# Kernel tuning notes

Measured on AMD Instinct MI355X. Metric: run time of the kernel, lower is better.

The kernel has to match this reference:

```python
import jax, jax.numpy as jnp
import numpy as np

B, N_DIM, K_DIM = 16384, 4096, 128


def setup_inputs() -> dict:
    key = jax.random.key(0)
    k1, k2, k3, k4 = jax.random.split(key, 4)
    x = jax.random.normal(k1, (B, N_DIM), dtype=jnp.float32)
    # nn.Linear(n_dim, 1): weight (1, n_dim), bias (1,)
    lim = 1.0 / np.sqrt(N_DIM)
    W = jax.random.uniform(k2, (1, N_DIM), dtype=jnp.float32, minval=-lim, maxval=lim)
    b = jax.random.uniform(k3, (1,), dtype=jnp.float32, minval=-lim, maxval=lim)
    # V initialized N(0, 0.001)
    V = 0.001 * jax.random.normal(k4, (N_DIM, K_DIM), dtype=jnp.float32)
    return {"x": x, "W": W, "b": b, "V": V}


def reference(x, W, b, V):
    # linear part: (B,1)
    linear = x @ W.T + b
    # term1 = 0.5 * sum_k (x @ V)_k^2  (torch code's 'sum_of_square')
    xv = x @ V  # (B, k)
    term1 = 0.5 * jnp.sum(xv * xv, axis=1, keepdims=True)
    # term2: torch's expand+matmul+bmm reduces algebraically to
    # -0.5 * (sum_i x_i)^2 * ||V.sum(0)||^2  (identical math, no (B,n,n) tensor)
    s = jnp.sum(V, axis=0)  # (k,)
    xsum = jnp.sum(x, axis=1, keepdims=True)  # (B,1)
    term2 = -0.5 * (xsum * xsum) * jnp.dot(s, s)
    return linear + term1 + term2
```

## Files before the change

### kernel.cpp

```cpp
#include <hip/hip_runtime.h>

typedef __bf16 bf16;
typedef __bf16 bf16x8 __attribute__((ext_vector_type(8)));
typedef float f32x16 __attribute__((ext_vector_type(16)));

#define B_ROWS 16384
#define N_DIM  4096
#define K_DIM  128

__global__ __launch_bounds__(256) void prep_kernel(const float* __restrict__ V,
                                                   float* __restrict__ spart,
                                                   bf16* __restrict__ Ut) {
    __shared__ bf16 tile[128 * 136];
    __shared__ float sp[256];
    const int t = threadIdx.x;
    const int jbase = blockIdx.x * 128;
    const int c  = t & 127;
    const int j0 = t >> 7;

    float sacc = 0.f;
#pragma unroll 8
    for (int i = 0; i < 64; ++i) {
        int j = j0 + 2 * i;
        float v = V[(size_t)(jbase + j) * K_DIM + c];
        sacc += v;
        tile[c * 136 + j] = (bf16)v;
    }
    sp[t] = sacc;
    __syncthreads();
    if (t < 128) spart[blockIdx.x * 128 + t] = sp[t] + sp[t + 128];

    const int col = t >> 1, half = t & 1;
#pragma unroll
    for (int i = 0; i < 4; ++i) {
        uint4 d = *(const uint4*)&tile[col * 136 + half * 64 + i * 16];
        *(uint4*)&Ut[(size_t)col * N_DIM + jbase + half * 64 + i * 16] = d;
    }
}

__global__ __launch_bounds__(128) void finalize_s(const float* __restrict__ spart,
                                                  float* __restrict__ snorm_out) {
    const int t = threadIdx.x;
    float s = 0.f;
#pragma unroll
    for (int b = 0; b < 32; ++b) s += spart[b * 128 + t];
    float sq = s * s;
#pragma unroll
    for (int m = 32; m >= 1; m >>= 1) sq += __shfl_down(sq, m, 64);
    __shared__ float red[2];
    if ((t & 63) == 0) red[t >> 6] = sq;
    __syncthreads();
    if (t == 0) snorm_out[0] = red[0] + red[1];
}

__global__ __launch_bounds__(256, 2) void fm_main(const float* __restrict__ x,
                                                  const float* __restrict__ W,
                                                  const float* __restrict__ bptr,
                                                  const bf16* __restrict__ Ut,
                                                  const float* __restrict__ snorm_ptr,
                                                  float* __restrict__ out) {
    __shared__ bf16  xs[32 * 72];
    __shared__ bf16  us[128 * 72];
    __shared__ float redxs[32 * 8];
    __shared__ float redxw[32 * 8];
    __shared__ float rowsq[4 * 32];

    const int t    = threadIdx.x;
    const int wave = t >> 6;
    const int lane = t & 63;
    const int l31  = lane & 31;
    const int h    = lane >> 5;
    const int r0   = blockIdx.x * 32;

    const int srow = t >> 3;
    const int scg  = t & 7;
    const int ucol = t >> 1;
    const int uhalf = t & 1;

    f32x16 acc;
#pragma unroll
    for (int i = 0; i < 16; ++i) acc[i] = 0.f;

    float xsum_acc = 0.f, xw_acc = 0.f;
    const float* xrow = x + (size_t)(r0 + srow) * N_DIM + scg * 8;
    const bf16*  urow = Ut + (size_t)ucol * N_DIM + uhalf * 32;

    for (int kb = 0; kb < N_DIM; kb += 64) {
        float4 a0 = *(const float4*)(xrow + kb);
        float4 a1 = *(const float4*)(xrow + kb + 4);
        float4 w0 = *(const float4*)(W + kb + scg * 8);
        float4 w1 = *(const float4*)(W + kb + scg * 8 + 4);
        const uint4* up = (const uint4*)(urow + kb);
        uint4 u0 = up[0], u1 = up[1], u2 = up[2], u3 = up[3];

        xsum_acc += (a0.x + a0.y + a0.z + a0.w) + (a1.x + a1.y + a1.z + a1.w);
        xw_acc   += a0.x * w0.x + a0.y * w0.y + a0.z * w0.z + a0.w * w0.w
                  + a1.x * w1.x + a1.y * w1.y + a1.z * w1.z + a1.w * w1.w;

        bf16x8 xb;
        xb[0] = (bf16)a0.x; xb[1] = (bf16)a0.y; xb[2] = (bf16)a0.z; xb[3] = (bf16)a0.w;
        xb[4] = (bf16)a1.x; xb[5] = (bf16)a1.y; xb[6] = (bf16)a1.z; xb[7] = (bf16)a1.w;

        __syncthreads();
        *(bf16x8*)&xs[srow * 72 + scg * 8] = xb;
        uint4* usp = (uint4*)&us[ucol * 72 + uhalf * 32];
        usp[0] = u0; usp[1] = u1; usp[2] = u2; usp[3] = u3;
        __syncthreads();

#pragma unroll
        for (int ks = 0; ks < 64; ks += 16) {
            bf16x8 af  = *(const bf16x8*)&xs[l31 * 72 + ks + h * 8];
            bf16x8 bfv = *(const bf16x8*)&us[(wave * 32 + l31) * 72 + ks + h * 8];
            acc = __builtin_amdgcn_mfma_f32_32x32x16_bf16(af, bfv, acc, 0, 0, 0);
        }
    }

    redxs[srow * 8 + scg] = xsum_acc;
    redxw[srow * 8 + scg] = xw_acc;

#pragma unroll
    for (int r = 0; r < 16; ++r) {
        float s = acc[r] * acc[r];
        s += __shfl_xor(s, 1);
        s += __shfl_xor(s, 2);
        s += __shfl_xor(s, 4);
        s += __shfl_xor(s, 8);
        s += __shfl_xor(s, 16);
        if (l31 == 0) {
            int row = (r & 3) + 8 * (r >> 2) + 4 * h;
            rowsq[wave * 32 + row] = s;
        }
    }
    __syncthreads();

    if (t < 32) {
        float xsum = 0.f, xw = 0.f;
#pragma unroll
        for (int g = 0; g < 8; ++g) { xsum += redxs[t * 8 + g]; xw += redxw[t * 8 + g]; }
        float sq = rowsq[t] + rowsq[32 + t] + rowsq[64 + t] + rowsq[96 + t];
        float snorm = snorm_ptr[0];
        float bv = bptr[0];
        out[r0 + t] = bv + xw + 0.5f * sq - 0.5f * xsum * xsum * snorm;
    }
}

extern "C" void kernel_launch(void* const* d_in, const int* in_sizes, int n_in,
                              void* d_out, int out_size, void* d_ws, size_t ws_size,
                              hipStream_t stream) {
    const float* x  = (const float*)d_in[0];
    const float* W  = (const float*)d_in[1];
    const float* bp = (const float*)d_in[2];
    const float* V  = (const float*)d_in[3];
    float* out = (float*)d_out;

    char* ws = (char*)d_ws;
    float* snorm = (float*)ws;
    float* spart = (float*)(ws + 1024);
    bf16*  Ut    = (bf16*)(ws + 32768);

    hipLaunchKernelGGL(prep_kernel, dim3(32), dim3(256), 0, stream, V, spart, Ut);
    hipLaunchKernelGGL(finalize_s, dim3(1), dim3(128), 0, stream, spart, snorm);
    hipLaunchKernelGGL(fm_main, dim3(512), dim3(256), 0, stream, x, W, bp, Ut, snorm, out);
}
```

Measured before the change: 399.8 us.

## Double-buffer LDS tiles and prefetch next x/U tile with direct-to-LDS loads

Converts the main GEMM loop to a double-buffered pipeline. The next x and W slices are prefetched into registers, and the next U tile is loaded straight into LDS with global_load_lds while MFMAs run on the current buffer. This cuts the two barriers per iteration to one and hides global memory latency behind compute. In exchange, the U tile in LDS loses its row padding, so MFMA operand reads may hit bank conflicts. Correctness also relies on the async LDS loads having completed before the barrier.

```diff
diff --git a/kernel.cpp b/kernel.cpp
--- a/kernel.cpp
+++ b/kernel.cpp
@@ -59,10 +59,10 @@
                                                   const bf16* __restrict__ Ut,
                                                   const float* __restrict__ snorm_ptr,
                                                   float* __restrict__ out) {
-    __shared__ bf16  xs[32 * 72];
-    __shared__ bf16  us[128 * 72];
-    __shared__ float redxs[32 * 8];
-    __shared__ float redxw[32 * 8];
+    __shared__ bf16  xs[2][32 * 72];
+    __shared__ bf16  us[2][128 * 64];
+    __shared__ float redxs[256];
+    __shared__ float redxw[256];
     __shared__ float rowsq[4 * 32];
 
     const int t    = threadIdx.x;
@@ -74,8 +74,6 @@
 
     const int srow = t >> 3;
     const int scg  = t & 7;
-    const int ucol = t >> 1;
-    const int uhalf = t & 1;
 
     f32x16 acc;
 #pragma unroll
@@ -83,40 +81,60 @@
 
     float xsum_acc = 0.f, xw_acc = 0.f;
     const float* xrow = x + (size_t)(r0 + srow) * N_DIM + scg * 8;
-    const bf16*  urow = Ut + (size_t)ucol * N_DIM + uhalf * 32;
+    const float* wrow = W + scg * 8;
+    const bf16* ub = Ut + (size_t)(wave * 32 + (lane >> 3)) * N_DIM + (lane & 7) * 8;
 
-    for (int kb = 0; kb < N_DIM; kb += 64) {
-        float4 a0 = *(const float4*)(xrow + kb);
-        float4 a1 = *(const float4*)(xrow + kb + 4);
-        float4 w0 = *(const float4*)(W + kb + scg * 8);
-        float4 w1 = *(const float4*)(W + kb + scg * 8 + 4);
-        const uint4* up = (const uint4*)(urow + kb);
-        uint4 u0 = up[0], u1 = up[1], u2 = up[2], u3 = up[3];
+    float4 a0 = *(const float4*)(xrow);
+    float4 a1 = *(const float4*)(xrow + 4);
+    float4 w0 = *(const float4*)(wrow);
+    float4 w1 = *(const float4*)(wrow + 4);
+#pragma unroll
+    for (int j = 0; j < 4; ++j) {
+        __builtin_amdgcn_global_load_lds(
+            (const __attribute__((address_space(1))) void*)(ub + (size_t)j * 8 * N_DIM),
+            (__attribute__((address_space(3))) void*)&us[0][(wave * 32 + j * 8) * 64],
+            16, 0, 0);
+    }
+
+    for (int it = 0; it < 64; ++it) {
+        const int b = it & 1;
+        const int kb_next = (it < 63) ? (it + 1) * 64 : 0;
+
+        bf16x8 xb;
+        xb[0] = (bf16)a0.x; xb[1] = (bf16)a0.y; xb[2] = (bf16)a0.z; xb[3] = (bf16)a0.w;
+        xb[4] = (bf16)a1.x; xb[5] = (bf16)a1.y; xb[6] = (bf16)a1.z; xb[7] = (bf16)a1.w;
+        *(bf16x8*)&xs[b][srow * 72 + scg * 8] = xb;
+
+        __syncthreads();
+
+        float4 na0 = *(const float4*)(xrow + kb_next);
+        float4 na1 = *(const float4*)(xrow + kb_next + 4);
+        float4 nw0 = *(const float4*)(wrow + kb_next);
+        float4 nw1 = *(const float4*)(wrow + kb_next + 4);
+#pragma unroll
+        for (int j = 0; j < 4; ++j) {
+            __builtin_amdgcn_global_load_lds(
+                (const __attribute__((address_space(1))) void*)(ub + (size_t)j * 8 * N_DIM + kb_next),
+                (__attribute__((address_space(3))) void*)&us[b ^ 1][(wave * 32 + j * 8) * 64],
+                16, 0, 0);
+        }
 
         xsum_acc += (a0.x + a0.y + a0.z + a0.w) + (a1.x + a1.y + a1.z + a1.w);
         xw_acc   += a0.x * w0.x + a0.y * w0.y + a0.z * w0.z + a0.w * w0.w
                   + a1.x * w1.x + a1.y * w1.y + a1.z * w1.z + a1.w * w1.w;
 
-        bf16x8 xb;
-        xb[0] = (bf16)a0.x; xb[1] = (bf16)a0.y; xb[2] = (bf16)a0.z; xb[3] = (bf16)a0.w;
-        xb[4] = (bf16)a1.x; xb[5] = (bf16)a1.y; xb[6] = (bf16)a1.z; xb[7] = (bf16)a1.w;
-
-        __syncthreads();
-        *(bf16x8*)&xs[srow * 72 + scg * 8] = xb;
-        uint4* usp = (uint4*)&us[ucol * 72 + uhalf * 32];
-        usp[0] = u0; usp[1] = u1; usp[2] = u2; usp[3] = u3;
-        __syncthreads();
-
 #pragma unroll
         for (int ks = 0; ks < 64; ks += 16) {
-            bf16x8 af  = *(const bf16x8*)&xs[l31 * 72 + ks + h * 8];
-            bf16x8 bfv = *(const bf16x8*)&us[(wave * 32 + l31) * 72 + ks + h * 8];
+            bf16x8 af  = *(const bf16x8*)&xs[b][l31 * 72 + ks + h * 8];
+            bf16x8 bfv = *(const bf16x8*)&us[b][(wave * 32 + l31) * 64 + ks + h * 8];
             acc = __builtin_amdgcn_mfma_f32_32x32x16_bf16(af, bfv, acc, 0, 0, 0);
         }
+
+        a0 = na0; a1 = na1; w0 = nw0; w1 = nw1;
     }
 
-    redxs[srow * 8 + scg] = xsum_acc;
-    redxw[srow * 8 + scg] = xw_acc;
+    redxs[t] = xsum_acc;
+    redxw[t] = xw_acc;
 
 #pragma unroll
     for (int r = 0; r < 16; ++r) {
```

After: 392.4 us. About the same (-1.9%).

## Load MFMA operands directly from global memory, dropping LDS staging and barriers

Applied to the files above, without the earlier changes.

The main kernel no longer stages x and U tiles through shared memory with two barriers per k-step. Each lane now loads its MFMA fragments directly from global memory into registers, and wave 0 alone computes the row sum and linear dot product. This removes LDS traffic and barriers from the loop. In exchange, every one of the four waves reads the same 32 rows of x, quadrupling x load requests that the cache must absorb, and the per-lane access pattern is strided across rows with less coalescing.

```diff
diff --git a/kernel.cpp b/kernel.cpp
--- a/kernel.cpp
+++ b/kernel.cpp
@@ -59,11 +59,9 @@
                                                   const bf16* __restrict__ Ut,
                                                   const float* __restrict__ snorm_ptr,
                                                   float* __restrict__ out) {
-    __shared__ bf16  xs[32 * 72];
-    __shared__ bf16  us[128 * 72];
-    __shared__ float redxs[32 * 8];
-    __shared__ float redxw[32 * 8];
     __shared__ float rowsq[4 * 32];
+    __shared__ float redx[32];
+    __shared__ float redw[32];
 
     const int t    = threadIdx.x;
     const int wave = t >> 6;
@@ -72,51 +70,48 @@
     const int h    = lane >> 5;
     const int r0   = blockIdx.x * 32;
 
-    const int srow = t >> 3;
-    const int scg  = t & 7;
-    const int ucol = t >> 1;
-    const int uhalf = t & 1;
-
     f32x16 acc;
 #pragma unroll
     for (int i = 0; i < 16; ++i) acc[i] = 0.f;
 
-    float xsum_acc = 0.f, xw_acc = 0.f;
-    const float* xrow = x + (size_t)(r0 + srow) * N_DIM + scg * 8;
-    const bf16*  urow = Ut + (size_t)ucol * N_DIM + uhalf * 32;
+    float xs_acc = 0.f, xw_acc = 0.f;
+
+    const float* xp = x + (size_t)(r0 + l31) * N_DIM + h * 8;
+    const bf16*  up = Ut + (size_t)(wave * 32 + l31) * N_DIM + h * 8;
+    const float* wp = W + h * 8;
 
     for (int kb = 0; kb < N_DIM; kb += 64) {
-        float4 a0 = *(const float4*)(xrow + kb);
-        float4 a1 = *(const float4*)(xrow + kb + 4);
-        float4 w0 = *(const float4*)(W + kb + scg * 8);
-        float4 w1 = *(const float4*)(W + kb + scg * 8 + 4);
-        const uint4* up = (const uint4*)(urow + kb);
-        uint4 u0 = up[0], u1 = up[1], u2 = up[2], u3 = up[3];
+        float4 xa0[4], xa1[4];
+        bf16x8 bfr[4];
+#pragma unroll
+        for (int j = 0; j < 4; ++j) {
+            xa0[j] = *(const float4*)(xp + kb + j * 16);
+            xa1[j] = *(const float4*)(xp + kb + j * 16 + 4);
+            bfr[j] = *(const bf16x8*)(up + kb + j * 16);
+        }
 
-        xsum_acc += (a0.x + a0.y + a0.z + a0.w) + (a1.x + a1.y + a1.z + a1.w);
-        xw_acc   += a0.x * w0.x + a0.y * w0.y + a0.z * w0.z + a0.w * w0.w
-                  + a1.x * w1.x + a1.y * w1.y + a1.z * w1.z + a1.w * w1.w;
-
-        bf16x8 xb;
-        xb[0] = (bf16)a0.x; xb[1] = (bf16)a0.y; xb[2] = (bf16)a0.z; xb[3] = (bf16)a0.w;
-        xb[4] = (bf16)a1.x; xb[5] = (bf16)a1.y; xb[6] = (bf16)a1.z; xb[7] = (bf16)a1.w;
-
-        __syncthreads();
-        *(bf16x8*)&xs[srow * 72 + scg * 8] = xb;
-        uint4* usp = (uint4*)&us[ucol * 72 + uhalf * 32];
-        usp[0] = u0; usp[1] = u1; usp[2] = u2; usp[3] = u3;
-        __syncthreads();
+        if (wave == 0) {
+#pragma unroll
+            for (int j = 0; j < 4; ++j) {
+                float4 w0 = *(const float4*)(wp + kb + j * 16);
+                float4 w1 = *(const float4*)(wp + kb + j * 16 + 4);
+                xs_acc += (xa0[j].x + xa0[j].y + xa0[j].z + xa0[j].w)
+                        + (xa1[j].x + xa1[j].y + xa1[j].z + xa1[j].w);
+                xw_acc += xa0[j].x * w0.x + xa0[j].y * w0.y + xa0[j].z * w0.z + xa0[j].w * w0.w
+                        + xa1[j].x * w1.x + xa1[j].y * w1.y + xa1[j].z * w1.z + xa1[j].w * w1.w;
+            }
+        }
 
 #pragma unroll
-        for (int ks = 0; ks < 64; ks += 16) {
-            bf16x8 af  = *(const bf16x8*)&xs[l31 * 72 + ks + h * 8];
-            bf16x8 bfv = *(const bf16x8*)&us[(wave * 32 + l31) * 72 + ks + h * 8];
-            acc = __builtin_amdgcn_mfma_f32_32x32x16_bf16(af, bfv, acc, 0, 0, 0);
+        for (int j = 0; j < 4; ++j) {
+            bf16x8 af;
+            af[0] = (bf16)xa0[j].x; af[1] = (bf16)xa0[j].y;
+            af[2] = (bf16)xa0[j].z; af[3] = (bf16)xa0[j].w;
+            af[4] = (bf16)xa1[j].x; af[5] = (bf16)xa1[j].y;
+            af[6] = (bf16)xa1[j].z; af[7] = (bf16)xa1[j].w;
+            acc = __builtin_amdgcn_mfma_f32_32x32x16_bf16(af, bfr[j], acc, 0, 0, 0);
         }
     }
-
-    redxs[srow * 8 + scg] = xsum_acc;
-    redxw[srow * 8 + scg] = xw_acc;
 
 #pragma unroll
     for (int r = 0; r < 16; ++r) {
@@ -126,21 +121,20 @@
         s += __shfl_xor(s, 4);
         s += __shfl_xor(s, 8);
         s += __shfl_xor(s, 16);
-        if (l31 == 0) {
-            int row = (r & 3) + 8 * (r >> 2) + 4 * h;
-            rowsq[wave * 32 + row] = s;
-        }
+        if (l31 == 0) rowsq[wave * 32 + ((r & 3) + 8 * (r >> 2) + 4 * h)] = s;
+    }
+
+    if (wave == 0) {
+        xs_acc += __shfl_xor(xs_acc, 32);
+        xw_acc += __shfl_xor(xw_acc, 32);
+        if (lane < 32) { redx[l31] = xs_acc; redw[l31] = xw_acc; }
     }
     __syncthreads();
 
     if (t < 32) {
-        float xsum = 0.f, xw = 0.f;
-#pragma unroll
-        for (int g = 0; g < 8; ++g) { xsum += redxs[t * 8 + g]; xw += redxw[t * 8 + g]; }
         float sq = rowsq[t] + rowsq[32 + t] + rowsq[64 + t] + rowsq[96 + t];
-        float snorm = snorm_ptr[0];
-        float bv = bptr[0];
-        out[r0 + t] = bv + xw + 0.5f * sq - 0.5f * xsum * xsum * snorm;
+        float xsum = redx[t];
+        out[r0 + t] = bptr[0] + redw[t] + 0.5f * sq - 0.5f * xsum * xsum * snorm_ptr[0];
     }
 }
 
```

New measurement: 488.3 us. 1.22x slower.
